# Kernel optimization log

Hardware: AMD Instinct MI355X
Metric: run time of the kernel (lower is better)

## Reference

```python
import jax, jax.numpy as jnp
import numpy as np

NV = [156, 618, 2466]     # vertices per ellipsoid level
NE = [462, 1848, 7392]    # edges per level
NGT = 30000               # ground-truth point-cloud size
LAP_CONST = [0.2, 1.0, 1.0]


def setup_inputs() -> dict:
    key = jax.random.key(0)
    ks = jax.random.split(key, 20)
    inp = {"points": jax.random.normal(ks[0], (1, NGT, 3), jnp.float32)}
    for i, (n, e) in enumerate(zip(NV, NE)):
        inp[f"pred_coord_{i}"] = jax.random.normal(ks[1 + i], (n, 3), jnp.float32)
        inp[f"pbd_{i}"] = jax.random.normal(ks[4 + i], (n, 3), jnp.float32)
        inp[f"edges_{i}"] = jax.random.randint(ks[7 + i], (e, 2), 0, n)
        # laplace_idx layout: 8 neighbor ids (-1 padded), vertex id, valence
        nbr = jax.random.randint(ks[10 + i], (n, 8), 0, n)
        drop = jax.random.uniform(ks[13 + i], (n, 8)) < 0.2
        drop = drop.at[:, 0].set(False)  # keep valence >= 1
        nbr = jnp.where(drop, -1, nbr)
        deg = (nbr >= 0).sum(1)
        inp[f"lap_idx_{i}"] = jnp.concatenate(
            [nbr, jnp.arange(n)[:, None], deg[:, None]], axis=1)
    return inp


def chamfer(gt, pred):
    # gt: [B, Ng, 3], pred: [B, Np, 3] -> squared NN distances each way
    d = (jnp.sum(gt * gt, -1)[:, :, None]
         + jnp.sum(pred * pred, -1)[:, None, :]
         - 2.0 * jnp.einsum('bnd,bmd->bnm', gt, pred))  # [B, Ng, Np]
    return jnp.min(d, axis=2), jnp.min(d, axis=1)


def edge_regularization(pred, edges):
    edge = pred[edges[:, 0]] - pred[edges[:, 1]]
    return jnp.mean(jnp.sum(edge * edge, axis=1)) * 300.0


def laplace_coord(x, lap_idx):
    nbr = lap_idx[:, :8]
    valid = nbr >= 0
    v = jnp.where(valid[:, :, None], x[jnp.clip(nbr, 0)], 0.0)  # [N, 8, 3]
    deg = lap_idx[:, -1].astype(x.dtype)
    return x - v.sum(1) / deg[:, None]


def laplace_regularization(x_before, x_after, lap_idx, use_move):
    lap1 = laplace_coord(x_before, lap_idx)
    lap2 = laplace_coord(x_after, lap_idx)
    d = lap1 - lap2
    loss = jnp.mean(d * d) * 3.0  # MSE over [N,3] scaled by last dim
    if use_move:
        m = x_before - x_after
        loss = loss + jnp.mean(m * m) * 3.0
    return loss


def reference(points, pred_coord_0, pred_coord_1, pred_coord_2,
              pbd_0, pbd_1, pbd_2,
              edges_0, edges_1, edges_2,
              lap_idx_0, lap_idx_1, lap_idx_2):
    pred_coord = [pred_coord_0, pred_coord_1, pred_coord_2]
    pbd = [pbd_0, pbd_1, pbd_2]
    edges = [edges_0, edges_1, edges_2]
    lap_idx = [lap_idx_0, lap_idx_1, lap_idx_2]

    chamfer_loss = 0.0
    edge_loss = 0.0
    lap_loss = 0.0
    for i in range(3):
        dist1, dist2 = chamfer(points, pbd[i][None])
        chamfer_loss = chamfer_loss + jnp.mean(dist1) + jnp.mean(dist2)
        edge_loss = edge_loss + edge_regularization(pred_coord[i], edges[i])
        lap_loss = lap_loss + LAP_CONST[i] * laplace_regularization(
            pbd[i], pred_coord[i], lap_idx[i], i > 0)
    loss = 100.0 * chamfer_loss + 0.1 * edge_loss + 0.3 * lap_loss
    return loss, chamfer_loss, edge_loss, lap_loss
```

## Files before the change

### kernel.cpp

```cpp
#include <hip/hip_runtime.h>

#define NGT 30000
#define GT_TILE 512
#define NBLK_G 59
#define PRANGE 128
#define NCHUNK 27
#define NPACK 3456
#define RB 128

typedef float v2f __attribute__((ext_vector_type(2)));

#define OFF_PREDPACK 0
#define OFF_GTMIN    13824
#define OFF_PREDMIN  103824
#define OFF_PARTIALS 107064
#define OFF_COUNTER  107576

__global__ __launch_bounds__(256) void pack_kernel(
    const float* __restrict__ pbd0,
    const float* __restrict__ pbd1,
    const float* __restrict__ pbd2,
    float4* __restrict__ predpack,
    float* __restrict__ gtmin,
    float* __restrict__ predmin,
    unsigned* __restrict__ counter)
{
    const int i = blockIdx.x * 256 + threadIdx.x;
    if (i == 0) *counter = 0u;
    if (i < 90000) gtmin[i] = __int_as_float(0x7f7f7f7f);
    else if (i < 93240) predmin[i - 90000] = __int_as_float(0x7f7f7f7f);
    if (i >= NPACK) return;
    int mesh, j, n;
    if (i < 256)      { mesh = 0; j = i;       n = 156; }
    else if (i < 896) { mesh = 1; j = i - 256; n = 618; }
    else              { mesh = 2; j = i - 896; n = 2466; }
    const float* p = (mesh == 0) ? pbd0 : (mesh == 1) ? pbd1 : pbd2;
    float4 v = make_float4(0.f, 0.f, 0.f, 3.0e38f);
    if (j < n) {
        float x = p[3*j], y = p[3*j+1], z = p[3*j+2];
        v = make_float4(x, y, z, x*x + y*y + z*z);
    }
    predpack[i] = v;
}

__global__ __launch_bounds__(256) void chamfer_kernel(
    const float* __restrict__ gt,
    const float4* __restrict__ predpack,
    float* __restrict__ gtmin,
    float* __restrict__ predmin)
{
    __shared__ float4 sgt[GT_TILE];
    __shared__ float4 spred[PRANGE];

    const int tid = threadIdx.x;
    const int c = blockIdx.y;

    int mesh, cidx;
    if (c < 2)      { mesh = 0; cidx = c; }
    else if (c < 7) { mesh = 1; cidx = c - 2; }
    else            { mesh = 2; cidx = c - 7; }
    const int coff = cidx * PRANGE;
    const int n    = (mesh == 0) ? 156 : (mesh == 1) ? 618 : 2466;
    const int poff = (mesh == 0) ? 0   : (mesh == 1) ? 156 : 774;
    const int pbase = ((mesh == 0) ? 0 : (mesh == 1) ? 256 : 896) + coff;
    const int np = min(PRANGE, n - coff);

    if (tid < PRANGE) spred[tid] = predpack[pbase + tid];

    const int gbase = blockIdx.x * GT_TILE;
    float gx[2], gy[2], gz[2], g2[2];
    #pragma unroll
    for (int k = 0; k < 2; ++k) {
        const int g = gbase + k * 256 + tid;
        float x = 1e18f, y = 1e18f, z = 1e18f;
        if (g < NGT) { x = gt[3*g]; y = gt[3*g+1]; z = gt[3*g+2]; }
        gx[k] = x; gy[k] = y; gz[k] = z;
        g2[k] = x*x + y*y + z*z;
        sgt[k * 256 + tid] = make_float4(x, y, z, g2[k]);
    }
    __syncthreads();

    {
        v2f gxv = {gx[0], gx[1]};
        v2f gyv = {gy[0], gy[1]};
        v2f gzv = {gz[0], gz[1]};
        v2f gminv = {3.0e38f, 3.0e38f};
        const float4* __restrict__ pp = predpack + pbase;
        #pragma unroll 8
        for (int j = 0; j < PRANGE; ++j) {
            const float4 p = pp[j];
            v2f dot = gxv * p.x;
            dot += gyv * p.y;
            dot += gzv * p.z;
            v2f t = dot * -2.0f + p.w;
            gminv.x = fminf(gminv.x, t.x);
            gminv.y = fminf(gminv.y, t.y);
        }
        int g = gbase + tid;
        if (g < NGT)
            atomicMin((int*)(gtmin + mesh * NGT + g),
                      __float_as_int(gminv.x + g2[0]));
        g += 256;
        if (g < NGT)
            atomicMin((int*)(gtmin + mesh * NGT + g),
                      __float_as_int(gminv.y + g2[1]));
    }

    {
        const int grp = tid >> 3;
        const int s   = tid & 7;
        const float4 P0 = spred[4*grp+0], P1 = spred[4*grp+1];
        const float4 P2 = spred[4*grp+2], P3 = spred[4*grp+3];
        v2f px01 = {P0.x, P1.x}, px23 = {P2.x, P3.x};
        v2f py01 = {P0.y, P1.y}, py23 = {P2.y, P3.y};
        v2f pz01 = {P0.z, P1.z}, pz23 = {P2.z, P3.z};
        v2f mn01 = {3.0e38f, 3.0e38f}, mn23 = {3.0e38f, 3.0e38f};
        #pragma unroll 4
        for (int k = 0; k < GT_TILE / 8; ++k) {
            const float4 q = sgt[k * 8 + s];
            v2f d01 = px01 * q.x; d01 += py01 * q.y; d01 += pz01 * q.z;
            v2f d23 = px23 * q.x; d23 += py23 * q.y; d23 += pz23 * q.z;
            v2f t01 = d01 * -2.0f + q.w;
            v2f t23 = d23 * -2.0f + q.w;
            mn01.x = fminf(mn01.x, t01.x); mn01.y = fminf(mn01.y, t01.y);
            mn23.x = fminf(mn23.x, t23.x); mn23.y = fminf(mn23.y, t23.y);
        }
        float mn[4] = {mn01.x, mn01.y, mn23.x, mn23.y};
        float pw[4] = {P0.w, P1.w, P2.w, P3.w};
        #pragma unroll
        for (int off = 1; off < 8; off <<= 1) {
            #pragma unroll
            for (int r = 0; r < 4; ++r)
                mn[r] = fminf(mn[r], __shfl_xor(mn[r], off, 64));
        }
        if (s == 0) {
            #pragma unroll
            for (int r = 0; r < 4; ++r) {
                const int pj = 4*grp + r;
                if (pj < np)
                    atomicMin((int*)(predmin + poff + coff + pj),
                              __float_as_int(mn[r] + pw[r]));
            }
        }
    }
}

__global__ __launch_bounds__(256) void partial_kernel(
    const float* __restrict__ pc0, const float* __restrict__ pc1, const float* __restrict__ pc2,
    const float* __restrict__ pbd0, const float* __restrict__ pbd1, const float* __restrict__ pbd2,
    const int* __restrict__ ed0, const int* __restrict__ ed1, const int* __restrict__ ed2,
    const int* __restrict__ li0, const int* __restrict__ li1, const int* __restrict__ li2,
    const float* __restrict__ gtmin, const float* __restrict__ predmin,
    float* __restrict__ partials, unsigned* __restrict__ counter,
    float* __restrict__ out)
{
    const int   NVs[3]   = {156, 618, 2466};
    const int   NEs[3]   = {462, 1848, 7392};
    const int   poffs[3] = {0, 156, 774};
    const int   eoffs[3] = {0, 462, 2310};
    const float lapc[3]  = {0.2f, 1.0f, 1.0f};
    const float* pcs[3]  = {pc0, pc1, pc2};
    const float* pbds[3] = {pbd0, pbd1, pbd2};
    const int*   eds[3]  = {ed0, ed1, ed2};
    const int*   lis[3]  = {li0, li1, li2};

    const int tid = threadIdx.x;
    const int stride = gridDim.x * 256;
    float ch = 0.f, ed = 0.f, lp = 0.f;

    for (int idx = blockIdx.x * 256 + tid; idx < 38682; idx += stride) {
        if (idx < 22500) {
            const float4 q = ((const float4*)gtmin)[idx];
            ch += (q.x + q.y + q.z + q.w) * (1.0f / 30000.0f);
        } else if (idx < 25740) {
            int p = idx - 22500;
            int m = (p < 156) ? 0 : (p < 774) ? 1 : 2;
            ch += predmin[p] * (1.0f / (float)NVs[m]);
        } else if (idx < 35442) {
            int e = idx - 25740;
            int m = (e < 462) ? 0 : (e < 2310) ? 1 : 2;
            int el = e - eoffs[m];
            const int* E = eds[m];
            const float* P = pcs[m];
            int a = E[2*el], b = E[2*el+1];
            float dx = P[3*a]   - P[3*b];
            float dy = P[3*a+1] - P[3*b+1];
            float dz = P[3*a+2] - P[3*b+2];
            ed += (dx*dx + dy*dy + dz*dz) * (300.0f / (float)NEs[m]);
        } else {
            int v = idx - 35442;
            int m = (v < 156) ? 0 : (v < 774) ? 1 : 2;
            int vl = v - poffs[m];
            const int* L = lis[m];
            const float* PB = pbds[m];
            const float* PC = pcs[m];
            float mvx = PB[3*vl]   - PC[3*vl];
            float mvy = PB[3*vl+1] - PC[3*vl+1];
            float mvz = PB[3*vl+2] - PC[3*vl+2];
            float sx = 0.f, sy = 0.f, sz = 0.f;
            #pragma unroll
            for (int k = 0; k < 8; ++k) {
                int nb = L[10*vl + k];
                if (nb >= 0) {
                    sx += PB[3*nb]   - PC[3*nb];
                    sy += PB[3*nb+1] - PC[3*nb+1];
                    sz += PB[3*nb+2] - PC[3*nb+2];
                }
            }
            float invdeg = 1.0f / (float)L[10*vl + 9];
            float dx = mvx - sx * invdeg;
            float dy = mvy - sy * invdeg;
            float dz = mvz - sz * invdeg;
            float t = dx*dx + dy*dy + dz*dz;
            if (m > 0) t += mvx*mvx + mvy*mvy + mvz*mvz;
            lp += t * (lapc[m] / (float)NVs[m]);
        }
    }

    __shared__ float sred[12];
    __shared__ int is_last;
    for (int off = 32; off; off >>= 1) {
        ch += __shfl_down(ch, off, 64);
        ed += __shfl_down(ed, off, 64);
        lp += __shfl_down(lp, off, 64);
    }
    const int lane = tid & 63, wid = tid >> 6;
    if (lane == 0) { sred[wid] = ch; sred[4 + wid] = ed; sred[8 + wid] = lp; }
    __syncthreads();
    if (tid == 0) {
        partials[blockIdx.x * 4 + 0] = sred[0] + sred[1] + sred[2] + sred[3];
        partials[blockIdx.x * 4 + 1] = sred[4] + sred[5] + sred[6] + sred[7];
        partials[blockIdx.x * 4 + 2] = sred[8] + sred[9] + sred[10] + sred[11];
        __threadfence();
        unsigned prev = atomicAdd(counter, 1u);
        is_last = (prev == (unsigned)(gridDim.x - 1)) ? 1 : 0;
    }
    __syncthreads();

    if (is_last) {
        __threadfence();
        float c2 = 0.f, e2 = 0.f, l2 = 0.f;
        if (tid < RB) {
            c2 = partials[4*tid]; e2 = partials[4*tid+1]; l2 = partials[4*tid+2];
        }
        for (int off = 32; off; off >>= 1) {
            c2 += __shfl_down(c2, off, 64);
            e2 += __shfl_down(e2, off, 64);
            l2 += __shfl_down(l2, off, 64);
        }
        __shared__ float s2[12];
        if (lane == 0) { s2[wid] = c2; s2[4 + wid] = e2; s2[8 + wid] = l2; }
        __syncthreads();
        if (tid == 0) {
            float C = s2[0] + s2[1];
            float E = s2[4] + s2[5];
            float L = s2[8] + s2[9];
            out[0] = 100.0f * C + 0.1f * E + 0.3f * L;
            out[1] = C;
            out[2] = E;
            out[3] = L;
        }
    }
}

extern "C" void kernel_launch(void* const* d_in, const int* in_sizes, int n_in,
                              void* d_out, int out_size, void* d_ws, size_t ws_size,
                              hipStream_t stream) {
    const float* gt   = (const float*)d_in[0];
    const float* pc0  = (const float*)d_in[1];
    const float* pbd0 = (const float*)d_in[2];
    const int*   ed0  = (const int*)  d_in[3];
    const int*   li0  = (const int*)  d_in[4];
    const float* pc1  = (const float*)d_in[5];
    const float* pbd1 = (const float*)d_in[6];
    const int*   ed1  = (const int*)  d_in[7];
    const int*   li1  = (const int*)  d_in[8];
    const float* pc2  = (const float*)d_in[9];
    const float* pbd2 = (const float*)d_in[10];
    const int*   ed2  = (const int*)  d_in[11];
    const int*   li2  = (const int*)  d_in[12];

    float* ws         = (float*)d_ws;
    float4* predpack  = (float4*)(ws + OFF_PREDPACK);
    float* gtmin      = ws + OFF_GTMIN;
    float* predmin    = ws + OFF_PREDMIN;
    float* partials   = ws + OFF_PARTIALS;
    unsigned* counter = (unsigned*)(ws + OFF_COUNTER);
    float* out        = (float*)d_out;

    pack_kernel<<<(93240 + 255) / 256, 256, 0, stream>>>(
        pbd0, pbd1, pbd2, predpack, gtmin, predmin, counter);

    dim3 grid(NBLK_G, NCHUNK);
    chamfer_kernel<<<grid, 256, 0, stream>>>(gt, predpack, gtmin, predmin);

    partial_kernel<<<RB, 256, 0, stream>>>(pc0, pc1, pc2, pbd0, pbd1, pbd2,
                                           ed0, ed1, ed2, li0, li1, li2,
                                           gtmin, predmin, partials, counter, out);
}
```

Before: 44.22 us.

## Broadcast gt points via readlane instead of LDS for pred-side chamfer min

```diff
diff --git a/kernel.cpp b/kernel.cpp
--- a/kernel.cpp
+++ b/kernel.cpp
@@ -15,6 +15,10 @@
 #define OFF_PREDMIN  103824
 #define OFF_PARTIALS 107064
 #define OFF_COUNTER  107576
+
+__device__ __forceinline__ float rdlane(float v, int k) {
+    return __int_as_float(__builtin_amdgcn_readlane(__float_as_int(v), k));
+}
 
 __global__ __launch_bounds__(256) void pack_kernel(
     const float* __restrict__ pbd0,
@@ -49,10 +53,8 @@
     float* __restrict__ gtmin,
     float* __restrict__ predmin)
 {
-    __shared__ float4 sgt[GT_TILE];
-    __shared__ float4 spred[PRANGE];
-
     const int tid = threadIdx.x;
+    const int lane = tid & 63;
     const int c = blockIdx.y;
 
     int mesh, cidx;
@@ -65,8 +67,6 @@
     const int pbase = ((mesh == 0) ? 0 : (mesh == 1) ? 256 : 896) + coff;
     const int np = min(PRANGE, n - coff);
 
-    if (tid < PRANGE) spred[tid] = predpack[pbase + tid];
-
     const int gbase = blockIdx.x * GT_TILE;
     float gx[2], gy[2], gz[2], g2[2];
     #pragma unroll
@@ -76,9 +76,7 @@
         if (g < NGT) { x = gt[3*g]; y = gt[3*g+1]; z = gt[3*g+2]; }
         gx[k] = x; gy[k] = y; gz[k] = z;
         g2[k] = x*x + y*y + z*z;
-        sgt[k * 256 + tid] = make_float4(x, y, z, g2[k]);
-    }
-    __syncthreads();
+    }
 
     {
         v2f gxv = {gx[0], gx[1]};
@@ -107,41 +105,35 @@
     }
 
     {
-        const int grp = tid >> 3;
-        const int s   = tid & 7;
-        const float4 P0 = spred[4*grp+0], P1 = spred[4*grp+1];
-        const float4 P2 = spred[4*grp+2], P3 = spred[4*grp+3];
-        v2f px01 = {P0.x, P1.x}, px23 = {P2.x, P3.x};
-        v2f py01 = {P0.y, P1.y}, py23 = {P2.y, P3.y};
-        v2f pz01 = {P0.z, P1.z}, pz23 = {P2.z, P3.z};
-        v2f mn01 = {3.0e38f, 3.0e38f}, mn23 = {3.0e38f, 3.0e38f};
+        const float4 P0 = predpack[pbase + 2*lane];
+        const float4 P1 = predpack[pbase + 2*lane + 1];
+        v2f px = {P0.x, P1.x};
+        v2f py = {P0.y, P1.y};
+        v2f pz = {P0.z, P1.z};
+        v2f mn = {3.0e38f, 3.0e38f};
         #pragma unroll 4
-        for (int k = 0; k < GT_TILE / 8; ++k) {
-            const float4 q = sgt[k * 8 + s];
-            v2f d01 = px01 * q.x; d01 += py01 * q.y; d01 += pz01 * q.z;
-            v2f d23 = px23 * q.x; d23 += py23 * q.y; d23 += pz23 * q.z;
-            v2f t01 = d01 * -2.0f + q.w;
-            v2f t23 = d23 * -2.0f + q.w;
-            mn01.x = fminf(mn01.x, t01.x); mn01.y = fminf(mn01.y, t01.y);
-            mn23.x = fminf(mn23.x, t23.x); mn23.y = fminf(mn23.y, t23.y);
-        }
-        float mn[4] = {mn01.x, mn01.y, mn23.x, mn23.y};
-        float pw[4] = {P0.w, P1.w, P2.w, P3.w};
-        #pragma unroll
-        for (int off = 1; off < 8; off <<= 1) {
+        for (int k = 0; k < 64; ++k) {
             #pragma unroll
-            for (int r = 0; r < 4; ++r)
-                mn[r] = fminf(mn[r], __shfl_xor(mn[r], off, 64));
-        }
-        if (s == 0) {
-            #pragma unroll
-            for (int r = 0; r < 4; ++r) {
-                const int pj = 4*grp + r;
-                if (pj < np)
-                    atomicMin((int*)(predmin + poff + coff + pj),
-                              __float_as_int(mn[r] + pw[r]));
+            for (int h = 0; h < 2; ++h) {
+                const float bx = rdlane(gx[h], k);
+                const float by = rdlane(gy[h], k);
+                const float bz = rdlane(gz[h], k);
+                const float b2 = rdlane(g2[h], k);
+                v2f dot = px * bx;
+                dot += py * by;
+                dot += pz * bz;
+                v2f t = dot * -2.0f + b2;
+                mn.x = fminf(mn.x, t.x);
+                mn.y = fminf(mn.y, t.y);
             }
         }
+        const int pj0 = 2*lane, pj1 = 2*lane + 1;
+        if (pj0 < np)
+            atomicMin((int*)(predmin + poff + coff + pj0),
+                      __float_as_int(mn.x + P0.w));
+        if (pj1 < np)
+            atomicMin((int*)(predmin + poff + coff + pj1),
+                      __float_as_int(mn.y + P1.w));
     }
 }
 
```

After: 62.85 us. 42.1% more time.
